# Performance work log

Measured on AMD Instinct MI355X. Metric: run time of the kernel, lower is better.

The kernel has to match this reference:

```python
import jax, jax.numpy as jnp
import numpy as np

B, S, E = 4, 2048, 1024


def setup_inputs() -> dict:
    key = jax.random.key(0)
    ks = jax.random.split(key, 7)
    s = 1.0 / np.sqrt(E)  # torch Linear default init scale (uniform bound)
    inp = {
        "input": jax.random.normal(ks[0], (B, S, E), dtype=jnp.float32),
        "masked": 1,
        "W_q": jax.random.uniform(ks[1], (E, E), jnp.float32, -s, s),
        "b_q": jax.random.uniform(ks[2], (E,), jnp.float32, -s, s),
        "W_k": jax.random.uniform(ks[3], (E, E), jnp.float32, -s, s),
        "b_k": jax.random.uniform(ks[4], (E,), jnp.float32, -s, s),
        "W_v": jax.random.uniform(ks[5], (E, E), jnp.float32, -s, s),
        "b_v": jax.random.uniform(ks[6], (E,), jnp.float32, -s, s),
    }
    return inp


def reference(input, masked, W_q, b_q, W_k, b_k, W_v, b_v):
    # torch.nn.Linear: y = x @ W.T + b
    q = jnp.einsum("bse,fe->bsf", input, W_q) + b_q
    k = jnp.einsum("bse,fe->bsf", input, W_k) + b_k
    v = jnp.einsum("bse,fe->bsf", input, W_v) + b_v
    d = q.shape[-1]
    scores = jnp.einsum("bqd,bkd->bqk", q, k) / jnp.sqrt(jnp.float32(d))
    if masked:
        Sq = scores.shape[1]
        causal = jnp.tril(jnp.ones((Sq, Sq), dtype=bool))  # [S,S], broadcast over batch
        scores = jnp.where(causal, scores, -jnp.inf)
    attn = jax.nn.softmax(scores, axis=-1)
    return jnp.einsum("bqk,bkd->bqd", attn, v)
```

## Files before the change

### kernel.cpp

```cpp
#include <hip/hip_runtime.h>

typedef _Float16 f16;
typedef f16 f16x8 __attribute__((ext_vector_type(8)));
typedef f16 f16x4v __attribute__((ext_vector_type(4)));
typedef float f32x4 __attribute__((ext_vector_type(4)));

__device__ __forceinline__ void async_ld16(const void* g, void* l) {
    __builtin_amdgcn_global_load_lds(
        (const __attribute__((address_space(1))) unsigned int*)g,
        (__attribute__((address_space(3))) unsigned int*)l, 16, 0, 0);
}


#define STG(b, op, kh, P, P1, tOff) do {                                        \
    char* d_ = (char*)smem + (b) * 65536 + (op) * 32768 + (kh) * 16384 + stgBase; \
    async_ld16((P)  + (tOff) * 64 + (kh) * 32, d_);                             \
    async_ld16((P1) + (tOff) * 64 + (kh) * 32, d_ + 8192);                      \
} while (0)
#define RD_A(b, kk) do {                                                        \
    const char* s_ = (const char*)smem + (b) * 65536 + (kk) * 16384 + aOff;     \
    _Pragma("unroll") for (int m_ = 0; m_ < 8; ++m_)                            \
        af[m_] = *(const f16x8*)(s_ + m_ * 1024);                               \
} while (0)
#define RD_B2(b, kk, n0_) do {                                                  \
    const char* s_ = (const char*)smem + (b) * 65536 + 32768 + (kk) * 16384 + bOff; \
    bf[(n0_)]     = *(const f16x8*)(s_ + ((n0_)) * 1024);                       \
    bf[(n0_) + 1] = *(const f16x8*)(s_ + ((n0_) + 1) * 1024);                   \
} while (0)
#define FENCE_MM(n0_) do {                                                      \
    __builtin_amdgcn_s_barrier();                                               \
    asm volatile("s_waitcnt lgkmcnt(0)" ::: "memory");                          \
    __builtin_amdgcn_sched_barrier(0);                                          \
    __builtin_amdgcn_s_setprio(1);                                              \
    _Pragma("unroll") for (int m_ = 0; m_ < 8; ++m_) {                          \
        acc[m_][(n0_)]     = __builtin_amdgcn_mfma_f32_16x16x32_f16(af[m_], bf[(n0_)],     acc[m_][(n0_)],     0, 0, 0); \
        acc[m_][(n0_) + 1] = __builtin_amdgcn_mfma_f32_16x16x32_f16(af[m_], bf[(n0_) + 1], acc[m_][(n0_) + 1], 0, 0, 0); \
    }                                                                           \
    __builtin_amdgcn_s_setprio(0);                                              \
} while (0)
#define VMC(n) asm volatile("s_waitcnt vmcnt(" #n ")" ::: "memory")
#define BAR __builtin_amdgcn_s_barrier()

#define GEMM256_MAIN_LOOP do {                                                  \
    STG(0, 0, 0, pA, pA1, 0); STG(0, 1, 0, pB, pB1, 0);                         \
    STG(0, 0, 1, pA, pA1, 0); STG(0, 1, 1, pB, pB1, 0);                         \
    STG(1, 0, 0, pA, pA1, 1); STG(1, 1, 0, pB, pB1, 1);                         \
    VMC(4);                                                                     \
    BAR;                                                                        \
    _Pragma("unroll 1")                                                         \
    for (int i_ = 0; i_ < 7; ++i_) {                                            \
        RD_A(0, 0); RD_B2(0, 0, 0); STG(1, 0, 1, pA, pA1, 1);           \
        FENCE_MM(0); BAR;                                                       \
        RD_B2(0, 0, 2);             STG(1, 1, 1, pB, pB1, 1);           \
        FENCE_MM(2); BAR;                                                       \
        RD_A(0, 1); RD_B2(0, 1, 0); STG(0, 0, 0, pA, pA1, 2);           \
        FENCE_MM(0); BAR;                                                       \
        RD_B2(0, 1, 2);             STG(0, 1, 0, pB, pB1, 2);           \
        FENCE_MM(2); VMC(4); BAR;                                               \
        RD_A(1, 0); RD_B2(1, 0, 0); STG(0, 0, 1, pA, pA1, 2);           \
        FENCE_MM(0); BAR;                                                       \
        RD_B2(1, 0, 2);             STG(0, 1, 1, pB, pB1, 2);           \
        FENCE_MM(2); BAR;                                                       \
        RD_A(1, 1); RD_B2(1, 1, 0); STG(1, 0, 0, pA, pA1, 3);           \
        FENCE_MM(0); BAR;                                                       \
        RD_B2(1, 1, 2);             STG(1, 1, 0, pB, pB1, 3);           \
        FENCE_MM(2); VMC(4); BAR;                                               \
        pA += 128; pA1 += 128; pB += 128; pB1 += 128;                           \
    }                                                                           \
    RD_A(0, 0); RD_B2(0, 0, 0); STG(1, 0, 1, pA, pA1, 1);                       \
    FENCE_MM(0); BAR;                                                           \
    RD_B2(0, 0, 2);             STG(1, 1, 1, pB, pB1, 1);                       \
    FENCE_MM(2); BAR;                                                           \
    RD_A(0, 1); RD_B2(0, 1, 0);                                                 \
    FENCE_MM(0); BAR;                                                           \
    RD_B2(0, 1, 2);                                                             \
    FENCE_MM(2); VMC(0); BAR;                                                   \
    RD_A(1, 0); RD_B2(1, 0, 0);                                                 \
    FENCE_MM(0); BAR;                                                           \
    RD_B2(1, 0, 2);                                                             \
    FENCE_MM(2); BAR;                                                           \
    RD_A(1, 1); RD_B2(1, 1, 0);                                                 \
    FENCE_MM(0); BAR;                                                           \
    RD_B2(1, 1, 2);                                                             \
    FENCE_MM(2); BAR;        \
} while (0)

#define GEMM256_SETUP                                                           \
    __shared__ __align__(16) f16 smem[65536];                      \
    const int tid = threadIdx.x;                                                \
    const int wave = tid >> 6, lane = tid & 63;                                 \
    const int wrow = wave >> 2, wcol = wave & 3;                                \
    const int quad = lane >> 4, l16 = lane & 15;                                \
    const int rowLane = tid >> 2;                                               \
    const int cOff = ((tid & 3) ^ ((tid >> 3) & 3)) * 8;                        \
    const int stgBase = wave * 1024;                                            \
    const int swz  = (quad ^ ((l16 >> 1) & 3)) * 16;                            \
    const int aOff = (wrow * 128 + l16) * 64 + swz;                             \
    const int bOff = (wcol * 64 + l16) * 64 + swz;                              \
    f32x4 acc[8][4];                                                            \
    _Pragma("unroll") for (int m_i = 0; m_i < 8; ++m_i)                         \
        _Pragma("unroll") for (int n_i = 0; n_i < 4; ++n_i)                     \
            acc[m_i][n_i] = (f32x4){0.f, 0.f, 0.f, 0.f};                        \
    f16x8 af[8], bf[4];

__global__ __launch_bounds__(512, 2) void qkv256(
    const f16* __restrict__ A, const f16* __restrict__ Bt,
    const float* __restrict__ b_q, const float* __restrict__ b_k,
    const float* __restrict__ b_v,
    f16* __restrict__ Q16, f16* __restrict__ K16, f16* __restrict__ Vt16)
{
    int bid = blockIdx.x;
    bid = (bid & 7) * 48 + (bid >> 3);
    const int by = bid / 12, bx = bid - by * 12;
    const int mBase = by * 256, nBase = bx * 256;

    GEMM256_SETUP

    const f16* pA  = A  + (long)(mBase + rowLane) * 1024 + cOff;
    const f16* pA1 = pA + 128 * 1024;
    const f16* pB  = Bt + (long)(nBase + rowLane) * 1024 + cOff;
    const f16* pB1 = pB + 128 * 1024;

    GEMM256_MAIN_LOOP;

    const int seg = nBase >> 10;
    const float* bs = (seg == 0) ? b_q : (seg == 1) ? b_k : b_v;
    const int lcb = (nBase & 1023) + wcol * 64;
    float bvv[4];
#pragma unroll
    for (int n = 0; n < 4; ++n) bvv[n] = bs[lcb + n * 16 + l16];

    if (seg < 2) {
        f16* dst = (seg == 0) ? Q16 : K16;
#pragma unroll
        for (int m = 0; m < 8; ++m)
#pragma unroll
            for (int n = 0; n < 4; ++n)
#pragma unroll
                for (int r = 0; r < 4; ++r) {
                    const int row = mBase + wrow * 128 + m * 16 + quad * 4 + r;
                    dst[(long)row * 1024 + lcb + n * 16 + l16] =
                        (f16)(acc[m][n][r] + bvv[n]);
                }
    } else {
        const int b = mBase >> 11, s0 = mBase & 2047;
        const int e0 = (nBase & 1023) + wcol * 64;
        f16* epiW = smem + wave * (64 * 80);
#pragma unroll
        for (int sb = 0; sb < 2; ++sb) {
#pragma unroll
            for (int m4 = 0; m4 < 4; ++m4)
#pragma unroll
                for (int n = 0; n < 4; ++n) {
                    f16x4v pk;
#pragma unroll
                    for (int r = 0; r < 4; ++r)
                        pk[r] = (f16)(acc[sb * 4 + m4][n][r] + bvv[n]);
                    *(f16x4v*)&epiW[(n * 16 + l16) * 80 + m4 * 16 + quad * 4] = pk;
                }
            asm volatile("s_waitcnt lgkmcnt(0)" ::: "memory");
#pragma unroll
            for (int it = 0; it < 8; ++it) {
                const int e = it * 8 + (lane >> 3);
                const f16x8 v = *(const f16x8*)&epiW[e * 80 + (lane & 7) * 8];
                *(f16x8*)(Vt16 + ((long)b * 1024 + e0 + e) * 2048 + s0 +
                          wrow * 128 + sb * 64 + (lane & 7) * 8) = v;
            }
        }
    }
}

__global__ __launch_bounds__(512, 2) void scores256(
    const f16* __restrict__ Q, const f16* __restrict__ K,
    f16* __restrict__ P, float* __restrict__ rowsum,
    const int* __restrict__ maskedp)
{
    const int masked = *maskedp;
    const int bx = blockIdx.x, by = blockIdx.y, bz = blockIdx.z;
    if (masked && bx > by) return;
    const int mBase = by * 256, nBase = bx * 256;

    GEMM256_SETUP

    const f16* Ab  = Q + (long)bz * (2048L * 1024);
    const f16* Btb = K + (long)bz * (2048L * 1024);
    const f16* pA  = Ab  + (long)(mBase + rowLane) * 1024 + cOff;
    const f16* pA1 = pA + 128 * 1024;
    const f16* pB  = Btb + (long)(nBase + rowLane) * 1024 + cOff;
    const f16* pB1 = pB + 128 * 1024;

    GEMM256_MAIN_LOOP;

    f16* Crow = P + (long)bz * (2048L * 2048);
    float* rsb = rowsum + bz * 2048;
#pragma unroll
    for (int m = 0; m < 8; ++m) {
        float rs[4] = {0.f, 0.f, 0.f, 0.f};
#pragma unroll
        for (int n = 0; n < 4; ++n)
#pragma unroll
            for (int r = 0; r < 4; ++r) {
                const int row = mBase + wrow * 128 + m * 16 + quad * 4 + r;
                const int col = nBase + wcol * 64 + n * 16 + l16;
                float e = __expf(acc[m][n][r] * 0.03125f);
                if (masked && col > row) e = 0.f;
                const f16 hv = (f16)e;
                Crow[(long)row * 2048 + col] = hv;
                rs[r] += (float)hv;
            }
#pragma unroll
        for (int r = 0; r < 4; ++r) {
            float s = rs[r];
            s += __shfl_xor(s, 1);
            s += __shfl_xor(s, 2);
            s += __shfl_xor(s, 4);
            s += __shfl_xor(s, 8);
            if (l16 == 0) {
                const int row = mBase + wrow * 128 + m * 16 + quad * 4 + r;
                atomicAdd(&rsb[row], s);
            }
        }
    }
}

#undef STG
#undef RD_A
#undef RD_B2
#undef FENCE_MM
#undef VMC
#undef BAR
#undef GEMM256_MAIN_LOOP
#undef GEMM256_SETUP

template <int MODE>
__global__ __launch_bounds__((MODE == 0) ? 256 : 512) void gemm_bt(
    const f16* __restrict__ A, long strideAb, int lda,
    const f16* __restrict__ Bt, long strideBb, int ldb,
    const float* __restrict__ b_q, const float* __restrict__ b_k,
    const float* __restrict__ b_v, float* __restrict__ rowsum,
    void* __restrict__ C0, void* __restrict__ C1, void* __restrict__ C2,
    long strideCb, int K,
    const int* __restrict__ maskedp)
{
    constexpr int NT  = (MODE == 0) ? 256 : 512;
    constexpr int NI  = (MODE == 0) ? 4 : 2;
    constexpr int RND = (128 * 32) / (NT * 8);

    const int bx = blockIdx.x, bz = blockIdx.z;
    const int by = (MODE >= 2) ? (gridDim.y - 1 - blockIdx.y) : blockIdx.y;
    const int masked = maskedp ? *maskedp : 1;
    if (MODE == 2 && masked && bx > by) return;
    int kmax = K;
    if (MODE == 3 && masked) kmax = min(K, (by + 1) * 128);

    A  += (long)bz * strideAb;
    Bt += (long)bz * strideBb;

    __shared__ __align__(16) f16 smem[256 * 64];
    f16* sA = smem;
    f16* sB = smem + 128 * 64;

    const int tid  = threadIdx.x;
    const int wave = tid >> 6, lane = tid & 63;
    const int wrow = wave >> 1, wcol = wave & 1;
    const int quad = lane >> 4, l16 = lane & 15;
    const int mBase = by * 128, nBase = bx * 128;

    f32x4 acc[NI][4];
#pragma unroll
    for (int i = 0; i < NI; ++i)
#pragma unroll
        for (int j = 0; j < 4; ++j)
            acc[i][j] = (f32x4){0.f, 0.f, 0.f, 0.f};

    const f16* aP[RND];
    const f16* bP[RND];
#pragma unroll
    for (int r = 0; r < RND; ++r) {
        aP[r] = A  + (long)(mBase + ((r * NT + tid) >> 2)) * lda + ((tid * 8) & 31);
        bP[r] = Bt + (long)(nBase + ((r * NT + tid) >> 2)) * ldb + ((tid * 8) & 31);
    }
    const int ldsOff = wave * 512;

    const int nT = kmax >> 6;
    for (int kt = 0; kt < nT; ++kt) {
#pragma unroll
        for (int h = 0; h < 2; ++h)
#pragma unroll
            for (int r = 0; r < RND; ++r) {
                async_ld16(aP[r] + h * 32, &sA[h * 4096 + r * (NT * 8) + ldsOff]);
                async_ld16(bP[r] + h * 32, &sB[h * 4096 + r * (NT * 8) + ldsOff]);
            }
#pragma unroll
        for (int r = 0; r < RND; ++r) { aP[r] += 64; bP[r] += 64; }
        __syncthreads();

#pragma unroll
        for (int h = 0; h < 2; ++h) {
            f16x8 af[NI], bf[4];
#pragma unroll
            for (int i = 0; i < NI; ++i)
                af[i] = *(const f16x8*)&sA[h * 4096 + (wrow * (16 * NI) + i * 16 + l16) * 32 + quad * 8];
#pragma unroll
            for (int j = 0; j < 4; ++j)
                bf[j] = *(const f16x8*)&sB[h * 4096 + (wcol * 64 + j * 16 + l16) * 32 + quad * 8];
#pragma unroll
            for (int i = 0; i < NI; ++i)
#pragma unroll
                for (int j = 0; j < 4; ++j)
                    acc[i][j] = __builtin_amdgcn_mfma_f32_16x16x32_f16(af[i], bf[j], acc[i][j], 0, 0, 0);
        }
        __syncthreads();
    }

    if (MODE == 2) {
        f16* Crow = (f16*)C0 + (long)bz * strideCb;
        float* rsb = rowsum + bz * 2048;
#pragma unroll
        for (int i = 0; i < NI; ++i) {
            float rs[4] = {0.f, 0.f, 0.f, 0.f};
#pragma unroll
            for (int j = 0; j < 4; ++j)
#pragma unroll
                for (int r = 0; r < 4; ++r) {
                    const int row = mBase + wrow * 32 + i * 16 + quad * 4 + r;
                    const int col = nBase + wcol * 64 + j * 16 + l16;
                    float e = __expf(acc[i][j][r] * 0.03125f);
                    if (masked && col > row) e = 0.f;
                    const f16 hv = (f16)e;
                    Crow[(long)row * 2048 + col] = hv;
                    rs[r] += (float)hv;
                }
#pragma unroll
            for (int r = 0; r < 4; ++r) {
                float s = rs[r];
                s += __shfl_xor(s, 1);
                s += __shfl_xor(s, 2);
                s += __shfl_xor(s, 4);
                s += __shfl_xor(s, 8);
                if (l16 == 0) {
                    const int row = mBase + wrow * 32 + i * 16 + quad * 4 + r;
                    atomicAdd(&rsb[row], s);
                }
            }
        }
    } else if (MODE == 3) {
        float* Crow = (float*)C0 + (long)bz * strideCb;
        const float* rsb = rowsum + bz * 2048;
#pragma unroll
        for (int i = 0; i < NI; ++i)
#pragma unroll
            for (int r = 0; r < 4; ++r) {
                const int row = mBase + wrow * 32 + i * 16 + quad * 4 + r;
                const float inv = 1.f / rsb[row];
#pragma unroll
                for (int j = 0; j < 4; ++j) {
                    const int col = nBase + wcol * 64 + j * 16 + l16;
                    Crow[(long)row * 1024 + col] = acc[i][j][r] * inv;
                }
            }
    }
}

__global__ void cvt_inp(const float* __restrict__ in, f16* __restrict__ out, int n4)
{
    const int i = blockIdx.x * blockDim.x + threadIdx.x;
    if (i >= n4) return;
    const float4 v = ((const float4*)in)[i];
    f16x4v o;
    o[0] = (f16)v.x; o[1] = (f16)v.y; o[2] = (f16)v.z; o[3] = (f16)v.w;
    ((f16x4v*)out)[i] = o;
}

__global__ void cvt_w3(const float* __restrict__ W0, const float* __restrict__ W1,
                       const float* __restrict__ W2, f16* __restrict__ out)
{
    const int bxx = blockIdx.x;
    const int which = bxx >> 10;
    const float* src = (which == 0) ? W0 : (which == 1) ? W1 : W2;
    const int i = (bxx & 1023) * 256 + threadIdx.x;
    const float4 v = ((const float4*)src)[i];
    f16x4v o;
    o[0] = (f16)v.x; o[1] = (f16)v.y; o[2] = (f16)v.z; o[3] = (f16)v.w;
    ((f16x4v*)(out + (long)which * 1024 * 1024))[i] = o;
}

extern "C" void kernel_launch(void* const* d_in, const int* in_sizes, int n_in,
                              void* d_out, int out_size, void* d_ws, size_t ws_size,
                              hipStream_t stream)
{
    const float* inp = (const float*)d_in[0];
    const int* masked = (const int*)d_in[1];
    const float* Wq = (const float*)d_in[2];
    const float* bq = (const float*)d_in[3];
    const float* Wk = (const float*)d_in[4];
    const float* bk = (const float*)d_in[5];
    const float* Wv = (const float*)d_in[6];
    const float* bv = (const float*)d_in[7];
    float* out = (float*)d_out;

    const int Bb = 4, S = 2048, E = 1024;
    const long nTok = (long)Bb * S;

    char* ws = (char*)d_ws;
    f16* inp16 = (f16*)ws;   ws += nTok * E * 2;
    f16* W3    = (f16*)ws;   ws += (long)3 * E * E * 2;
    f16* Q16   = (f16*)ws;   ws += nTok * E * 2;
    f16* K16   = (f16*)ws;   ws += nTok * E * 2;
    f16* Vt16  = (f16*)ws;   ws += nTok * E * 2;
    f16* P16   = (f16*)ws;   ws += (long)Bb * S * S * 2;
    float* rsum = (float*)ws; ws += nTok * 4;

    dim3 blk(256);

    hipMemsetAsync(rsum, 0, nTok * 4, stream);
    cvt_inp<<<(int)(nTok * E / 4 / 256), blk, 0, stream>>>(inp, inp16, (int)(nTok * E / 4));
    cvt_w3<<<3 * 1024, blk, 0, stream>>>(Wq, Wk, Wv, W3);

    qkv256<<<dim3(32 * 12), dim3(512), 0, stream>>>(
        inp16, W3, bq, bk, bv, Q16, K16, Vt16);

    scores256<<<dim3(8, 8, 4), dim3(512), 0, stream>>>(
        Q16, K16, P16, rsum, masked);

    gemm_bt<3><<<dim3(E / 128, S / 128, Bb), dim3(512), 0, stream>>>(
        P16, (long)S * S, S, Vt16, (long)E * S, S, nullptr, nullptr, nullptr, rsum,
        out, nullptr, nullptr, (long)S * E, S, masked);
}
```

Baseline: 244.2 us.

## Replace generic P·V GEMM with pipelined 256x128 tile kernel

New measurement: 240.3 us. Within noise of the previous version (-1.6%).

```diff
diff --git a/kernel.cpp b/kernel.cpp
--- a/kernel.cpp
+++ b/kernel.cpp
@@ -227,140 +227,123 @@
 #undef RD_A
 #undef RD_B2
 #undef FENCE_MM
+#undef GEMM256_MAIN_LOOP
+#undef GEMM256_SETUP
+
+#define PSTG_A(b, kh, tOff) do {                                                \
+    char* d_ = (char*)smem + (b) * 49152 + (kh) * 16384 + stgBase;              \
+    async_ld16(pA  + (tOff) * 64 + (kh) * 32, d_);                              \
+    async_ld16(pA1 + (tOff) * 64 + (kh) * 32, d_ + 8192);                       \
+} while (0)
+#define PSTG_B(b, kh, tOff) do {                                                \
+    char* d_ = (char*)smem + (b) * 49152 + 32768 + (kh) * 8192 + stgBase;       \
+    async_ld16(pB + (tOff) * 64 + (kh) * 32, d_);                               \
+} while (0)
+#define PRD(b, kk) do {                                                         \
+    const char* sa_ = (const char*)smem + (b) * 49152 + (kk) * 16384 + aOff;    \
+    _Pragma("unroll") for (int m_ = 0; m_ < 8; ++m_)                            \
+        af[m_] = *(const f16x8*)(sa_ + m_ * 1024);                              \
+    const char* sb_ = (const char*)smem + (b) * 49152 + 32768 + (kk) * 8192 + bOff; \
+    bf[0] = *(const f16x8*)(sb_);                                               \
+    bf[1] = *(const f16x8*)(sb_ + 1024);                                        \
+} while (0)
+#define PFENCE do {                                                             \
+    __builtin_amdgcn_s_barrier();                                               \
+    asm volatile("s_waitcnt lgkmcnt(0)" ::: "memory");                          \
+    __builtin_amdgcn_sched_barrier(0);                                          \
+    __builtin_amdgcn_s_setprio(1);                                              \
+    _Pragma("unroll") for (int m_ = 0; m_ < 8; ++m_) {                          \
+        acc[m_][0] = __builtin_amdgcn_mfma_f32_16x16x32_f16(af[m_], bf[0], acc[m_][0], 0, 0, 0); \
+        acc[m_][1] = __builtin_amdgcn_mfma_f32_16x16x32_f16(af[m_], bf[1], acc[m_][1], 0, 0, 0); \
+    }                                                                           \
+    __builtin_amdgcn_s_setprio(0);                                              \
+} while (0)
+
+__global__ __launch_bounds__(512, 2) void pv256(
+    const f16* __restrict__ P, const f16* __restrict__ Vt,
+    const float* __restrict__ rowsum, float* __restrict__ out,
+    const int* __restrict__ maskedp)
+{
+    const int masked = *maskedp;
+    const int bx = blockIdx.x, by = blockIdx.y, bz = blockIdx.z;
+    const int mBase = by * 256, nBase = bx * 128;
+    const int nIter = masked ? (by + 1) * 2 : 16;
+
+    __shared__ __align__(16) f16 smem[49152];
+    const int tid = threadIdx.x;
+    const int wave = tid >> 6, lane = tid & 63;
+    const int wrow = wave >> 2, wcol = wave & 3;
+    const int quad = lane >> 4, l16 = lane & 15;
+    const int rowLane = tid >> 2;
+    const int cOff = ((tid & 3) ^ ((tid >> 3) & 3)) * 8;
+    const int stgBase = wave * 1024;
+    const int swz  = (quad ^ ((l16 >> 1) & 3)) * 16;
+    const int aOff = (wrow * 128 + l16) * 64 + swz;
+    const int bOff = (wcol * 32 + l16) * 64 + swz;
+
+    const f16* Pb = P  + (long)bz * (2048L * 2048);
+    const f16* Vb = Vt + (long)bz * (1024L * 2048);
+    const f16* pA  = Pb + (long)(mBase + rowLane) * 2048 + cOff;
+    const f16* pA1 = pA + 128 * 2048;
+    const f16* pB  = Vb + (long)(nBase + rowLane) * 2048 + cOff;
+
+    f32x4 acc[8][2];
+#pragma unroll
+    for (int m = 0; m < 8; ++m) {
+        acc[m][0] = (f32x4){0.f, 0.f, 0.f, 0.f};
+        acc[m][1] = (f32x4){0.f, 0.f, 0.f, 0.f};
+    }
+    f16x8 af[8], bf[2];
+
+    PSTG_A(0, 0, 0); PSTG_B(0, 0, 0);
+    PSTG_A(0, 1, 0); PSTG_B(0, 1, 0);
+    PSTG_A(1, 0, 1); PSTG_B(1, 0, 1);
+    VMC(3);
+    BAR;
+
+#pragma unroll 1
+    for (int i = 0; i < nIter - 1; ++i) {
+        PRD(0, 0); PSTG_A(1, 1, 1); PSTG_B(1, 1, 1);
+        PFENCE; VMC(6); BAR;
+        PRD(0, 1); PSTG_A(0, 0, 2); PSTG_B(0, 0, 2);
+        PFENCE; VMC(6); BAR;
+        PRD(1, 0); PSTG_A(0, 1, 2); PSTG_B(0, 1, 2);
+        PFENCE; VMC(6); BAR;
+        PRD(1, 1); PSTG_A(1, 0, 3); PSTG_B(1, 0, 3);
+        PFENCE; VMC(6); BAR;
+        pA += 128; pA1 += 128; pB += 128;
+    }
+    PRD(0, 0); PSTG_A(1, 1, 1); PSTG_B(1, 1, 1);
+    PFENCE; VMC(6); BAR;
+    PRD(0, 1);
+    PFENCE; VMC(3); BAR;
+    PRD(1, 0);
+    PFENCE; VMC(0); BAR;
+    PRD(1, 1);
+    PFENCE;
+
+    const float* rsb = rowsum + bz * 2048;
+    float* ob = out + (long)bz * (2048L * 1024);
+#pragma unroll
+    for (int m = 0; m < 8; ++m)
+#pragma unroll
+        for (int r = 0; r < 4; ++r) {
+            const int row = mBase + wrow * 128 + m * 16 + quad * 4 + r;
+            const float inv = 1.f / rsb[row];
+#pragma unroll
+            for (int n = 0; n < 2; ++n) {
+                const int col = nBase + wcol * 32 + n * 16 + l16;
+                ob[(long)row * 1024 + col] = acc[m][n][r] * inv;
+            }
+        }
+}
+
+#undef PSTG_A
+#undef PSTG_B
+#undef PRD
+#undef PFENCE
 #undef VMC
 #undef BAR
-#undef GEMM256_MAIN_LOOP
-#undef GEMM256_SETUP
-
-template <int MODE>
-__global__ __launch_bounds__((MODE == 0) ? 256 : 512) void gemm_bt(
-    const f16* __restrict__ A, long strideAb, int lda,
-    const f16* __restrict__ Bt, long strideBb, int ldb,
-    const float* __restrict__ b_q, const float* __restrict__ b_k,
-    const float* __restrict__ b_v, float* __restrict__ rowsum,
-    void* __restrict__ C0, void* __restrict__ C1, void* __restrict__ C2,
-    long strideCb, int K,
-    const int* __restrict__ maskedp)
-{
-    constexpr int NT  = (MODE == 0) ? 256 : 512;
-    constexpr int NI  = (MODE == 0) ? 4 : 2;
-    constexpr int RND = (128 * 32) / (NT * 8);
-
-    const int bx = blockIdx.x, bz = blockIdx.z;
-    const int by = (MODE >= 2) ? (gridDim.y - 1 - blockIdx.y) : blockIdx.y;
-    const int masked = maskedp ? *maskedp : 1;
-    if (MODE == 2 && masked && bx > by) return;
-    int kmax = K;
-    if (MODE == 3 && masked) kmax = min(K, (by + 1) * 128);
-
-    A  += (long)bz * strideAb;
-    Bt += (long)bz * strideBb;
-
-    __shared__ __align__(16) f16 smem[256 * 64];
-    f16* sA = smem;
-    f16* sB = smem + 128 * 64;
-
-    const int tid  = threadIdx.x;
-    const int wave = tid >> 6, lane = tid & 63;
-    const int wrow = wave >> 1, wcol = wave & 1;
-    const int quad = lane >> 4, l16 = lane & 15;
-    const int mBase = by * 128, nBase = bx * 128;
-
-    f32x4 acc[NI][4];
-#pragma unroll
-    for (int i = 0; i < NI; ++i)
-#pragma unroll
-        for (int j = 0; j < 4; ++j)
-            acc[i][j] = (f32x4){0.f, 0.f, 0.f, 0.f};
-
-    const f16* aP[RND];
-    const f16* bP[RND];
-#pragma unroll
-    for (int r = 0; r < RND; ++r) {
-        aP[r] = A  + (long)(mBase + ((r * NT + tid) >> 2)) * lda + ((tid * 8) & 31);
-        bP[r] = Bt + (long)(nBase + ((r * NT + tid) >> 2)) * ldb + ((tid * 8) & 31);
-    }
-    const int ldsOff = wave * 512;
-
-    const int nT = kmax >> 6;
-    for (int kt = 0; kt < nT; ++kt) {
-#pragma unroll
-        for (int h = 0; h < 2; ++h)
-#pragma unroll
-            for (int r = 0; r < RND; ++r) {
-                async_ld16(aP[r] + h * 32, &sA[h * 4096 + r * (NT * 8) + ldsOff]);
-                async_ld16(bP[r] + h * 32, &sB[h * 4096 + r * (NT * 8) + ldsOff]);
-            }
-#pragma unroll
-        for (int r = 0; r < RND; ++r) { aP[r] += 64; bP[r] += 64; }
-        __syncthreads();
-
-#pragma unroll
-        for (int h = 0; h < 2; ++h) {
-            f16x8 af[NI], bf[4];
-#pragma unroll
-            for (int i = 0; i < NI; ++i)
-                af[i] = *(const f16x8*)&sA[h * 4096 + (wrow * (16 * NI) + i * 16 + l16) * 32 + quad * 8];
-#pragma unroll
-            for (int j = 0; j < 4; ++j)
-                bf[j] = *(const f16x8*)&sB[h * 4096 + (wcol * 64 + j * 16 + l16) * 32 + quad * 8];
-#pragma unroll
-            for (int i = 0; i < NI; ++i)
-#pragma unroll
-                for (int j = 0; j < 4; ++j)
-                    acc[i][j] = __builtin_amdgcn_mfma_f32_16x16x32_f16(af[i], bf[j], acc[i][j], 0, 0, 0);
-        }
-        __syncthreads();
-    }
-
-    if (MODE == 2) {
-        f16* Crow = (f16*)C0 + (long)bz * strideCb;
-        float* rsb = rowsum + bz * 2048;
-#pragma unroll
-        for (int i = 0; i < NI; ++i) {
-            float rs[4] = {0.f, 0.f, 0.f, 0.f};
-#pragma unroll
-            for (int j = 0; j < 4; ++j)
-#pragma unroll
-                for (int r = 0; r < 4; ++r) {
-                    const int row = mBase + wrow * 32 + i * 16 + quad * 4 + r;
-                    const int col = nBase + wcol * 64 + j * 16 + l16;
-                    float e = __expf(acc[i][j][r] * 0.03125f);
-                    if (masked && col > row) e = 0.f;
-                    const f16 hv = (f16)e;
-                    Crow[(long)row * 2048 + col] = hv;
-                    rs[r] += (float)hv;
-                }
-#pragma unroll
-            for (int r = 0; r < 4; ++r) {
-                float s = rs[r];
-                s += __shfl_xor(s, 1);
-                s += __shfl_xor(s, 2);
-                s += __shfl_xor(s, 4);
-                s += __shfl_xor(s, 8);
-                if (l16 == 0) {
-                    const int row = mBase + wrow * 32 + i * 16 + quad * 4 + r;
-                    atomicAdd(&rsb[row], s);
-                }
-            }
-        }
-    } else if (MODE == 3) {
-        float* Crow = (float*)C0 + (long)bz * strideCb;
-        const float* rsb = rowsum + bz * 2048;
-#pragma unroll
-        for (int i = 0; i < NI; ++i)
-#pragma unroll
-            for (int r = 0; r < 4; ++r) {
-                const int row = mBase + wrow * 32 + i * 16 + quad * 4 + r;
-                const float inv = 1.f / rsb[row];
-#pragma unroll
-                for (int j = 0; j < 4; ++j) {
-                    const int col = nBase + wcol * 64 + j * 16 + l16;
-                    Crow[(long)row * 1024 + col] = acc[i][j][r] * inv;
-                }
-            }
-    }
-}
 
 __global__ void cvt_inp(const float* __restrict__ in, f16* __restrict__ out, int n4)
 {
@@ -423,7 +406,6 @@
     scores256<<<dim3(8, 8, 4), dim3(512), 0, stream>>>(
         Q16, K16, P16, rsum, masked);
 
-    gemm_bt<3><<<dim3(E / 128, S / 128, Bb), dim3(512), 0, stream>>>(
-        P16, (long)S * S, S, Vt16, (long)E * S, S, nullptr, nullptr, nullptr, rsum,
-        out, nullptr, nullptr, (long)S * E, S, masked);
-}
+    pv256<<<dim3(8, 8, 4), dim3(512), 0, stream>>>(
+        P16, Vt16, rsum, out, masked);
+}
```
